# Performance work log

Hardware: AMD Instinct MI355X
Metric: run time of the kernel (lower is better)

The kernel has to match this reference:

```python
import jax, jax.numpy as jnp
import numpy as np

N_IN = 100_000
N_OUT = 800_000
K = 27          # 3x3x3 kernel offsets
C_IN = 32
C_OUT = 64


def setup_inputs() -> dict:
    key = jax.random.key(0)
    k1, k2, k3, k4, k5, k6 = jax.random.split(key, 6)
    feats = jax.random.normal(k1, (N_IN, C_IN), dtype=jnp.float32)
    weight = jax.random.normal(k2, (K, C_IN, C_OUT), dtype=jnp.float32) * (1.0 / np.sqrt(C_IN * K))
    bias = jax.random.normal(k3, (C_OUT,), dtype=jnp.float32) * 0.01
    # bwd is the inverse sort permutation cached by the paired downsampling conv
    bwd = jax.random.permutation(k4, N_IN).astype(jnp.int64)
    # rulebook: per kernel offset, (input row, output row) pairs
    in_idx = jax.random.randint(k5, (K, N_IN), 0, N_IN, dtype=jnp.int64)
    out_idx = jax.random.randint(k6, (K, N_IN), 0, N_OUT, dtype=jnp.int64)
    return {"feats": feats, "weight": weight, "bias": bias,
            "bwd": bwd, "in_idx": in_idx, "out_idx": out_idx, "n_out": N_OUT}


def reference(feats, weight, bias, bwd, in_idx, out_idx, n_out):
    # 1) recover original feature order (the x.feats[bwd] gather)
    f = feats[bwd]                                   # [N_in, C_in]
    # 2) rulebook gather-GEMM-scatter
    gathered = f[in_idx]                             # [K, P, C_in]
    contrib = jnp.einsum('kpc,kcd->kpd', gathered, weight)  # [K, P, C_out]
    out = jnp.zeros((n_out, C_OUT), dtype=feats.dtype)
    out = out.at[out_idx].add(contrib)               # scatter-add over rulebook
    out = out + bias
    return out
```

## Files before the change

kernel.cpp:

```cpp
#include <hip/hip_runtime.h>

#define C_IN  32
#define C_OUT 64
#define KK    27

using frag_ab = __attribute__((ext_vector_type(8))) short;
using frag_cd = __attribute__((ext_vector_type(4))) float;
using u32x4   = __attribute__((ext_vector_type(4))) unsigned int;

static __device__ inline unsigned short f2bf(float f) {
    unsigned u = __float_as_uint(f);
    return (unsigned short)((u + 0x7fffu + ((u >> 16) & 1u)) >> 16);
}
static __device__ inline unsigned pack2(float a, float b) {
    return (unsigned)f2bf(a) | ((unsigned)f2bf(b) << 16);
}
static __device__ inline float bflo(unsigned u) { return __uint_as_float(u << 16); }
static __device__ inline float bfhi(unsigned u) { return __uint_as_float(u & 0xffff0000u); }

__global__ __launch_bounds__(256) void sic_init_bias(float4* __restrict__ out4,
                                                     const float4* __restrict__ bias4,
                                                     int total4) {
    int idx = blockIdx.x * 256 + threadIdx.x, stride = gridDim.x * 256;
    for (int i = idx; i < total4; i += stride) out4[i] = bias4[i & 15];
}

__global__ __launch_bounds__(256) void sic_scatter(
    const float* __restrict__ feats, const float* __restrict__ weight,
    const int* __restrict__ bwd, const int* __restrict__ in_idx,
    const int* __restrict__ out_idx, float* __restrict__ out, int n_in)
{
    const int k = blockIdx.y, lane = threadIdx.x & 63, wid = threadIdx.x >> 6;
    float w[C_IN];
    const float* wk = weight + k * (C_IN * C_OUT);
#pragma unroll
    for (int i = 0; i < C_IN; ++i) w[i] = wk[i * C_OUT + lane];
    const int waves_total = gridDim.x * 4;
    const long long base = (long long)k * n_in;
    for (int p = blockIdx.x * 4 + wid; p < n_in; p += waves_total) {
        int src = __builtin_amdgcn_readfirstlane(in_idx[base + p]);
        int dst = __builtin_amdgcn_readfirstlane(out_idx[base + p]);
        int row = __builtin_amdgcn_readfirstlane(bwd[src]);
        const float* f = feats + (long long)row * C_IN;
        float acc = 0.0f;
#pragma unroll
        for (int i = 0; i < C_IN; ++i) acc = fmaf(f[i], w[i], acc);
        atomicAdd(out + (long long)dst * C_OUT + lane, acc);
    }
}

__global__ __launch_bounds__(512) void sic_zero(int* __restrict__ p, int n) {
    int i = blockIdx.x * 512 + threadIdx.x, stride = gridDim.x * 512;
    for (; i < n; i += stride) p[i] = 0;
}

__global__ __launch_bounds__(256) void sic_fconv(const float* __restrict__ feats,
                                                 short* __restrict__ featsbf, int n_in) {
    int t = blockIdx.x * 256 + threadIdx.x;
    if (t >= (n_in + 1) * 4) return;
    int row = t >> 2, c8 = (t & 3) * 8;
    uint4 v = {0u, 0u, 0u, 0u};
    if (row < n_in) {
        const float* fp = feats + (size_t)row * C_IN + c8;
        float4 f0 = ((const float4*)fp)[0];
        float4 f1 = ((const float4*)fp)[1];
        v.x = pack2(f0.x, f0.y);
        v.y = pack2(f0.z, f0.w);
        v.z = pack2(f1.x, f1.y);
        v.w = pack2(f1.z, f1.w);
    }
    ((uint4*)featsbf)[t] = v;
}

__global__ __launch_bounds__(256) void sic_wconv(const float* __restrict__ weight,
                                                 short* __restrict__ wfrag) {
    int t = blockIdx.x * 256 + threadIdx.x;
    if (t >= KK * 4 * 64) return;
    int l = t & 63, nb = (t >> 6) & 3, k = t >> 8;
    int g = l >> 4, cl = l & 15;
    const float* wp = weight + (size_t)k * (C_IN * C_OUT) + nb * 16 + cl;
    float r[8];
#pragma unroll
    for (int j = 0; j < 8; ++j) r[j] = wp[(size_t)(g * 8 + j) * C_OUT];
    uint4 v = {pack2(r[0], r[1]), pack2(r[2], r[3]), pack2(r[4], r[5]), pack2(r[6], r[7])};
    ((uint4*)wfrag)[t] = v;
}

__global__ __launch_bounds__(256) void sic_hist3(const int* __restrict__ out_idx_seg,
                                                 int* __restrict__ count,
                                                 int* __restrict__ ord, int pseg) {
    int i = blockIdx.x * 256 + threadIdx.x;
    if (i < pseg) {
        ord[i] = atomicAdd(&count[out_idx_seg[i]], 1);
    }
}

__global__ __launch_bounds__(512) void sic_scanA(const int* __restrict__ in,
                                                 int* __restrict__ outExcl,
                                                 int* __restrict__ sums, int n) {
    __shared__ int sm[512];
    int tid = threadIdx.x;
    int base = blockIdx.x * 2048 + tid * 4;
    int e0 = (base + 0 < n) ? in[base + 0] : 0;
    int e1 = (base + 1 < n) ? in[base + 1] : 0;
    int e2 = (base + 2 < n) ? in[base + 2] : 0;
    int e3 = (base + 3 < n) ? in[base + 3] : 0;
    int s = e0 + e1 + e2 + e3;
    sm[tid] = s;
    __syncthreads();
    for (int off = 1; off < 512; off <<= 1) {
        int t = (tid >= off) ? sm[tid - off] : 0;
        __syncthreads();
        sm[tid] += t;
        __syncthreads();
    }
    int pre = sm[tid] - s;
    if (base + 0 < n) outExcl[base + 0] = pre;
    if (base + 1 < n) outExcl[base + 1] = pre + e0;
    if (base + 2 < n) outExcl[base + 2] = pre + e0 + e1;
    if (base + 3 < n) outExcl[base + 3] = pre + e0 + e1 + e2;
    if (tid == 511) sums[blockIdx.x] = sm[511];
}

__global__ __launch_bounds__(512) void sic_scan_small(int* __restrict__ buf, int n) {
    __shared__ int sm[512];
    int tid = threadIdx.x;
    int e = (tid < n) ? buf[tid] : 0;
    sm[tid] = e;
    __syncthreads();
    for (int off = 1; off < 512; off <<= 1) {
        int t = (tid >= off) ? sm[tid - off] : 0;
        __syncthreads();
        sm[tid] += t;
        __syncthreads();
    }
    if (tid < n) buf[tid] = sm[tid] - e;
}

__global__ __launch_bounds__(512) void sic_addbackA(int* __restrict__ arr,
                                                    const int* __restrict__ sums, int n) {
    int s = sums[blockIdx.x];
    int base = blockIdx.x * 2048 + threadIdx.x * 4;
#pragma unroll
    for (int i = 0; i < 4; ++i)
        if (base + i < n) arr[base + i] += s;
}

__global__ __launch_bounds__(256) void sic_gemm4(
    const int* __restrict__ in_idx,
    const int* __restrict__ out_idx,
    const int* __restrict__ bwd,
    const int* __restrict__ ord,
    const int* __restrict__ startv,
    const short* __restrict__ featsbf,
    const short* __restrict__ wfrag,
    unsigned int* __restrict__ contribU,
    int n_in, int k0, int zrow)
{
    const int kk   = k0 + blockIdx.y;
    const int lane = threadIdx.x & 63;
    const int wid  = threadIdx.x >> 6;
    const int g = lane >> 4, cl = lane & 15;

    const frag_ab wa0 = *(const frag_ab*)(wfrag + ((size_t)(kk * 4 + 0) * 64 + lane) * 8);
    const frag_ab wa1 = *(const frag_ab*)(wfrag + ((size_t)(kk * 4 + 1) * 64 + lane) * 8);
    const frag_ab wa2 = *(const frag_ab*)(wfrag + ((size_t)(kk * 4 + 2) * 64 + lane) * 8);
    const frag_ab wa3 = *(const frag_ab*)(wfrag + ((size_t)(kk * 4 + 3) * 64 + lane) * 8);
    const frag_cd zf = {0.f, 0.f, 0.f, 0.f};

    const size_t gk  = (size_t)kk * n_in;
    const size_t sk  = (size_t)blockIdx.y * n_in;
    const int t      = blockIdx.x * 4 + wid;
    const int idx    = t * 16 + cl;
    const bool valid = idx < n_in;

    int row = zrow, pos = 0;
    if (valid) {
        row = bwd[in_idx[gk + idx]];
        int dst = out_idx[gk + idx];
        pos = startv[dst] + ord[sk + idx];
    }

    frag_ab b = *(const frag_ab*)(featsbf + (size_t)row * C_IN + g * 8);
    frag_cd d0 = __builtin_amdgcn_mfma_f32_16x16x32_bf16(wa0, b, zf, 0, 0, 0);
    frag_cd d1 = __builtin_amdgcn_mfma_f32_16x16x32_bf16(wa1, b, zf, 0, 0, 0);
    frag_cd d2 = __builtin_amdgcn_mfma_f32_16x16x32_bf16(wa2, b, zf, 0, 0, 0);
    frag_cd d3 = __builtin_amdgcn_mfma_f32_16x16x32_bf16(wa3, b, zf, 0, 0, 0);

    if (valid) {
        unsigned int* cp = contribU + (size_t)pos * 32 + g * 8;
        uint4 v0 = {pack2(d0[0], d0[1]), pack2(d0[2], d0[3]),
                    pack2(d1[0], d1[1]), pack2(d1[2], d1[3])};
        uint4 v1 = {pack2(d2[0], d2[1]), pack2(d2[2], d2[3]),
                    pack2(d3[0], d3[1]), pack2(d3[2], d3[3])};
        *(uint4*)(cp)     = v0;
        *(uint4*)(cp + 4) = v1;
    }
}

__global__ __launch_bounds__(256) void sic_reduce5(
    const unsigned int* __restrict__ contribU,
    const int* __restrict__ startv, const int* __restrict__ count,
    const float* __restrict__ bias, float* __restrict__ out,
    int n_out, int first)
{
    int t = blockIdx.x * 256 + threadIdx.x;
    int dst = t >> 3, c8 = t & 7;
    if (dst >= n_out) return;
    int s = startv[dst], c = count[dst];

    const int chA = (c8 & 1) * 32 + (c8 >> 1) * 4;
    size_t obA = (size_t)dst * C_OUT + chA;
    size_t obB = obA + 16;
    float4 a0, a1;
    if (first) {
        a0 = *(const float4*)(bias + chA);
        a1 = *(const float4*)(bias + chA + 16);
    } else {
        a0 = *(const float4*)(out + obA);
        a1 = *(const float4*)(out + obB);
    }
    const u32x4* p = (const u32x4*)(contribU + (size_t)s * 32) + c8;
    int j = 0;
    for (; j + 2 <= c; j += 2) {
        u32x4 va = __builtin_nontemporal_load(&p[(size_t)j * 8]);
        u32x4 vb = __builtin_nontemporal_load(&p[(size_t)(j + 1) * 8]);
        a0.x += bflo(va.x); a0.y += bfhi(va.x);
        a0.z += bflo(va.y); a0.w += bfhi(va.y);
        a1.x += bflo(va.z); a1.y += bfhi(va.z);
        a1.z += bflo(va.w); a1.w += bfhi(va.w);
        a0.x += bflo(vb.x); a0.y += bfhi(vb.x);
        a0.z += bflo(vb.y); a0.w += bfhi(vb.y);
        a1.x += bflo(vb.z); a1.y += bfhi(vb.z);
        a1.z += bflo(vb.w); a1.w += bfhi(vb.w);
    }
    if (j < c) {
        u32x4 va = __builtin_nontemporal_load(&p[(size_t)j * 8]);
        a0.x += bflo(va.x); a0.y += bfhi(va.x);
        a0.z += bflo(va.y); a0.w += bfhi(va.y);
        a1.x += bflo(va.z); a1.y += bfhi(va.z);
        a1.z += bflo(va.w); a1.w += bfhi(va.w);
    }
    *(float4*)(out + obA) = a0;
    *(float4*)(out + obB) = a1;
}

extern "C" void kernel_launch(void* const* d_in, const int* in_sizes, int n_in_cnt,
                              void* d_out, int out_size, void* d_ws, size_t ws_size,
                              hipStream_t stream) {
    const float* feats   = (const float*)d_in[0];
    const float* weight  = (const float*)d_in[1];
    const float* bias    = (const float*)d_in[2];
    const int*   bwd     = (const int*)d_in[3];
    const int*   in_idx  = (const int*)d_in[4];
    const int*   out_idx = (const int*)d_in[5];
    float*       out     = (float*)d_out;

    const int n_in  = in_sizes[0] / C_IN;
    const int n_out = out_size / C_OUT;
    const size_t P  = (size_t)KK * n_in;

    const int NCHA = (n_out + 2047) / 2048;

    const size_t NOUTr   = ((size_t)n_out + 255) & ~(size_t)255;
    const size_t o_cnt   = 0;
    const size_t o_stv   = NOUTr;
    const size_t o_s1    = 2 * NOUTr;
    const size_t o_ord   = (o_s1 + 512 + 255) & ~(size_t)255;
    const size_t o_fbf   = (o_ord + P + 255) & ~(size_t)255;
    const size_t fbf_i   = ((size_t)(n_in + 16) * C_IN * 2 + 3) / 4;
    const size_t o_wfr   = (o_fbf + fbf_i + 255) & ~(size_t)255;
    const size_t wfr_i   = (size_t)KK * 4 * 64 * 8 * 2 / 4;
    const size_t o_ctr   = (o_wfr + wfr_i + 255) & ~(size_t)255;

    const size_t ws_ints = ws_size / 4;
    size_t cap_recs = (ws_ints > o_ctr) ? (ws_ints - o_ctr) / 32 : 0;
    int kseg_max = (int)(cap_recs / (size_t)n_in);
    if (kseg_max > KK) kseg_max = KK;

    if (kseg_max < 1 || NCHA > 512) {
        const int total4 = out_size / 4;
        hipLaunchKernelGGL(sic_init_bias, dim3(2048), dim3(256), 0, stream,
                           (float4*)out, (const float4*)bias, total4);
        hipLaunchKernelGGL(sic_scatter, dim3(160, KK), dim3(256), 0, stream,
                           feats, weight, bwd, in_idx, out_idx, out, n_in);
        return;
    }

    int* ws = (int*)d_ws;
    int* count  = ws + o_cnt;
    int* startv = ws + o_stv;
    int* sums   = ws + o_s1;
    int* ord    = ws + o_ord;
    short* featsbf = (short*)(ws + o_fbf);
    short* wfrag   = (short*)(ws + o_wfr);
    unsigned int* contribU = (unsigned int*)(ws + o_ctr);

    hipLaunchKernelGGL(sic_fconv, dim3(((n_in + 1) * 4 + 255) / 256), dim3(256), 0, stream,
                       feats, featsbf, n_in);
    hipLaunchKernelGGL(sic_wconv, dim3((KK * 4 * 64 + 255) / 256), dim3(256), 0, stream,
                       weight, wfrag);

    const int ntiles  = (n_in + 15) / 16;
    const int gx_gemm = (ntiles + 3) / 4;

    for (int k0 = 0; k0 < KK; k0 += kseg_max) {
        const int kseg = (KK - k0 < kseg_max) ? (KK - k0) : kseg_max;
        const int pseg = kseg * n_in;
        const int gp   = (pseg + 255) / 256;
        const int* oseg = out_idx + (size_t)k0 * n_in;

        hipLaunchKernelGGL(sic_zero, dim3(1024), dim3(512), 0, stream, count, n_out);
        hipLaunchKernelGGL(sic_hist3, dim3(gp), dim3(256), 0, stream,
                           oseg, count, ord, pseg);
        hipLaunchKernelGGL(sic_scanA, dim3(NCHA), dim3(512), 0, stream,
                           count, startv, sums, n_out);
        hipLaunchKernelGGL(sic_scan_small, dim3(1), dim3(512), 0, stream, sums, NCHA);
        hipLaunchKernelGGL(sic_addbackA, dim3(NCHA), dim3(512), 0, stream,
                           startv, sums, n_out);
        hipLaunchKernelGGL(sic_gemm4, dim3(gx_gemm, kseg), dim3(256), 0, stream,
                           in_idx, out_idx, bwd, ord, startv,
                           featsbf, wfrag, contribU, n_in, k0, n_in);
        hipLaunchKernelGGL(sic_reduce5, dim3((n_out * 8 + 255) / 256), dim3(256), 0, stream,
                           contribU, startv, count, bias, out,
                           n_out, (k0 == 0) ? 1 : 0);
    }
}
```

Measured before the change: 393.3 us.

## Stage GEMM outputs through LDS for row-contiguous stores; reduce with 32 lanes per row

```diff
diff --git a/kernel.cpp b/kernel.cpp
--- a/kernel.cpp
+++ b/kernel.cpp
@@ -6,7 +6,6 @@
 
 using frag_ab = __attribute__((ext_vector_type(8))) short;
 using frag_cd = __attribute__((ext_vector_type(4))) float;
-using u32x4   = __attribute__((ext_vector_type(4))) unsigned int;
 
 static __device__ inline unsigned short f2bf(float f) {
     unsigned u = __float_as_uint(f);
@@ -146,7 +145,7 @@
         if (base + i < n) arr[base + i] += s;
 }
 
-__global__ __launch_bounds__(256) void sic_gemm4(
+__global__ __launch_bounds__(256) void sic_gemm5(
     const int* __restrict__ in_idx,
     const int* __restrict__ out_idx,
     const int* __restrict__ bwd,
@@ -157,6 +156,7 @@
     unsigned int* __restrict__ contribU,
     int n_in, int k0, int zrow)
 {
+    __shared__ unsigned smU[4][16][40];
     const int kk   = k0 + blockIdx.y;
     const int lane = threadIdx.x & 63;
     const int wid  = threadIdx.x >> 6;
@@ -171,7 +171,8 @@
     const size_t gk  = (size_t)kk * n_in;
     const size_t sk  = (size_t)blockIdx.y * n_in;
     const int t      = blockIdx.x * 4 + wid;
-    const int idx    = t * 16 + cl;
+    const int tbase  = t * 16;
+    const int idx    = tbase + cl;
     const bool valid = idx < n_in;
 
     int row = zrow, pos = 0;
@@ -187,62 +188,59 @@
     frag_cd d2 = __builtin_amdgcn_mfma_f32_16x16x32_bf16(wa2, b, zf, 0, 0, 0);
     frag_cd d3 = __builtin_amdgcn_mfma_f32_16x16x32_bf16(wa3, b, zf, 0, 0, 0);
 
-    if (valid) {
-        unsigned int* cp = contribU + (size_t)pos * 32 + g * 8;
-        uint4 v0 = {pack2(d0[0], d0[1]), pack2(d0[2], d0[3]),
-                    pack2(d1[0], d1[1]), pack2(d1[2], d1[3])};
-        uint4 v1 = {pack2(d2[0], d2[1]), pack2(d2[2], d2[3]),
-                    pack2(d3[0], d3[1]), pack2(d3[2], d3[3])};
-        *(uint4*)(cp)     = v0;
-        *(uint4*)(cp + 4) = v1;
-    }
-}
-
-__global__ __launch_bounds__(256) void sic_reduce5(
+    {
+        uint2 v0 = {pack2(d0[0], d0[1]), pack2(d0[2], d0[3])};
+        uint2 v1 = {pack2(d1[0], d1[1]), pack2(d1[2], d1[3])};
+        uint2 v2 = {pack2(d2[0], d2[1]), pack2(d2[2], d2[3])};
+        uint2 v3 = {pack2(d3[0], d3[1]), pack2(d3[2], d3[3])};
+        *(uint2*)&smU[wid][cl][ 0 + g * 2] = v0;
+        *(uint2*)&smU[wid][cl][ 8 + g * 2] = v1;
+        *(uint2*)&smU[wid][cl][16 + g * 2] = v2;
+        *(uint2*)&smU[wid][cl][24 + g * 2] = v3;
+    }
+
+#pragma unroll
+    for (int p2 = 0; p2 < 2; ++p2) {
+        int r = (lane >> 3) + p2 * 8;
+        int c = lane & 7;
+        uint4 v = {smU[wid][r][c * 4 + 0], smU[wid][r][c * 4 + 1],
+                   smU[wid][r][c * 4 + 2], smU[wid][r][c * 4 + 3]};
+        int pos_r = __shfl(pos, r, 64);
+        if (tbase + r < n_in) {
+            *(uint4*)(contribU + (size_t)pos_r * 32 + c * 4) = v;
+        }
+    }
+}
+
+__global__ __launch_bounds__(256) void sic_reduce6(
     const unsigned int* __restrict__ contribU,
     const int* __restrict__ startv, const int* __restrict__ count,
     const float* __restrict__ bias, float* __restrict__ out,
     int n_out, int first)
 {
-    int t = blockIdx.x * 256 + threadIdx.x;
-    int dst = t >> 3, c8 = t & 7;
+    int wave = (blockIdx.x * 256 + threadIdx.x) >> 6;
+    int l = threadIdx.x & 63;
+    int h = l >> 5, q = l & 31;
+    int dst = wave * 2 + h;
     if (dst >= n_out) return;
     int s = startv[dst], c = count[dst];
-
-    const int chA = (c8 & 1) * 32 + (c8 >> 1) * 4;
-    size_t obA = (size_t)dst * C_OUT + chA;
-    size_t obB = obA + 16;
-    float4 a0, a1;
+    int ch = q * 2;
+
+    float a0, a1;
     if (first) {
-        a0 = *(const float4*)(bias + chA);
-        a1 = *(const float4*)(bias + chA + 16);
+        float2 bv = *(const float2*)(bias + ch);
+        a0 = bv.x; a1 = bv.y;
     } else {
-        a0 = *(const float4*)(out + obA);
-        a1 = *(const float4*)(out + obB);
-    }
-    const u32x4* p = (const u32x4*)(contribU + (size_t)s * 32) + c8;
-    int j = 0;
-    for (; j + 2 <= c; j += 2) {
-        u32x4 va = __builtin_nontemporal_load(&p[(size_t)j * 8]);
-        u32x4 vb = __builtin_nontemporal_load(&p[(size_t)(j + 1) * 8]);
-        a0.x += bflo(va.x); a0.y += bfhi(va.x);
-        a0.z += bflo(va.y); a0.w += bfhi(va.y);
-        a1.x += bflo(va.z); a1.y += bfhi(va.z);
-        a1.z += bflo(va.w); a1.w += bfhi(va.w);
-        a0.x += bflo(vb.x); a0.y += bfhi(vb.x);
-        a0.z += bflo(vb.y); a0.w += bfhi(vb.y);
-        a1.x += bflo(vb.z); a1.y += bfhi(vb.z);
-        a1.z += bflo(vb.w); a1.w += bfhi(vb.w);
-    }
-    if (j < c) {
-        u32x4 va = __builtin_nontemporal_load(&p[(size_t)j * 8]);
-        a0.x += bflo(va.x); a0.y += bfhi(va.x);
-        a0.z += bflo(va.y); a0.w += bfhi(va.y);
-        a1.x += bflo(va.z); a1.y += bfhi(va.z);
-        a1.z += bflo(va.w); a1.w += bfhi(va.w);
-    }
-    *(float4*)(out + obA) = a0;
-    *(float4*)(out + obB) = a1;
+        float2 ov = *(const float2*)(out + (size_t)dst * C_OUT + ch);
+        a0 = ov.x; a1 = ov.y;
+    }
+    const unsigned int* p = contribU + (size_t)s * 32 + q;
+    for (int j = 0; j < c; ++j) {
+        unsigned u = __builtin_nontemporal_load(p + (size_t)j * 32);
+        a0 += bflo(u); a1 += bfhi(u);
+    }
+    float2 v = {a0, a1};
+    *(float2*)(out + (size_t)dst * C_OUT + ch) = v;
 }
 
 extern "C" void kernel_launch(void* const* d_in, const int* in_sizes, int n_in_cnt,
@@ -304,6 +302,9 @@
     const int ntiles  = (n_in + 15) / 16;
     const int gx_gemm = (ntiles + 3) / 4;
 
+    const int nwaves_red = (n_out + 1) / 2;
+    const int gx_red = (nwaves_red + 3) / 4;
+
     for (int k0 = 0; k0 < KK; k0 += kseg_max) {
         const int kseg = (KK - k0 < kseg_max) ? (KK - k0) : kseg_max;
         const int pseg = kseg * n_in;
@@ -318,10 +319,10 @@
         hipLaunchKernelGGL(sic_scan_small, dim3(1), dim3(512), 0, stream, sums, NCHA);
         hipLaunchKernelGGL(sic_addbackA, dim3(NCHA), dim3(512), 0, stream,
                            startv, sums, n_out);
-        hipLaunchKernelGGL(sic_gemm4, dim3(gx_gemm, kseg), dim3(256), 0, stream,
+        hipLaunchKernelGGL(sic_gemm5, dim3(gx_gemm, kseg), dim3(256), 0, stream,
                            in_idx, out_idx, bwd, ord, startv,
                            featsbf, wfrag, contribU, n_in, k0, n_in);
-        hipLaunchKernelGGL(sic_reduce5, dim3((n_out * 8 + 255) / 256), dim3(256), 0, stream,
+        hipLaunchKernelGGL(sic_reduce6, dim3(gx_red), dim3(256), 0, stream,
                            contribU, startv, count, bias, out,
                            n_out, (k0 == 0) ? 1 : 0);
     }
```

New measurement: 481.1 us. +22.3%, slower.
